# Performance work log

Hardware: AMD Instinct MI355X
Metric: run time of the kernel (lower is better)

## Reference

```python
import jax, jax.numpy as jnp
import numpy as np
from jax import lax

T, B, IN, H, L = 512, 64, 512, 1024, 2


def setup_inputs() -> dict:
    key = jax.random.key(0)
    ks = jax.random.split(key, 2 + 4 * L)
    inp = {
        'input_': jax.random.normal(ks[0], (T, B, IN), dtype=jnp.float32),
        # binary float mask for variable-length sequences
        'mask': (jax.random.uniform(ks[1], (T, B)) > 0.2).astype(jnp.float32),
    }
    k = 1.0 / np.sqrt(H)  # torch LSTMCell init range
    sizes = [(IN, H), (H, H)]
    for l in range(L):
        li, _ = sizes[l]
        base = 2 + 4 * l
        inp[f'Wih{l}'] = jax.random.uniform(ks[base + 0], (4 * H, li), minval=-k, maxval=k)
        inp[f'Whh{l}'] = jax.random.uniform(ks[base + 1], (4 * H, H), minval=-k, maxval=k)
        inp[f'bih{l}'] = jax.random.uniform(ks[base + 2], (4 * H,), minval=-k, maxval=k)
        inp[f'bhh{l}'] = jax.random.uniform(ks[base + 3], (4 * H,), minval=-k, maxval=k)
    return inp


def _lstm_layer(x, mask, Wih, Whh, bih, bhh):
    # x: [T,B,di], mask: [T,B]; precompute input-side gates for all steps
    xg = jnp.einsum('tbd,gd->tbg', x, Wih) + bih + bhh  # [T,B,4H]
    Bn = x.shape[1]
    h0 = jnp.zeros((Bn, Whh.shape[1]), x.dtype)
    c0 = jnp.zeros_like(h0)

    def step(carry, inp):
        h, c = carry
        g_x, m = inp
        gates = g_x + h @ Whh.T  # [B,4H]
        i, f, g, o = jnp.split(gates, 4, axis=-1)
        c_new = jax.nn.sigmoid(f) * c + jax.nn.sigmoid(i) * jnp.tanh(g)
        h_new = jax.nn.sigmoid(o) * jnp.tanh(c_new)
        m = m[:, None]
        h_new = h_new * m + h * (1.0 - m)
        c_new = c_new * m + c * (1.0 - m)
        return (h_new, c_new), h_new

    (h_n, c_n), out = lax.scan(step, (h0, c0), (xg, mask))
    return out, h_n, c_n


def reference(input_, mask, Wih0, Whh0, bih0, bhh0, Wih1, Whh1, bih1, bhh1):
    params = [(Wih0, Whh0, bih0, bhh0), (Wih1, Whh1, bih1, bhh1)]
    x = input_
    h_list, c_list = [], []
    for Wih, Whh, bih, bhh in params:
        x, h_n, c_n = _lstm_layer(x, mask, Wih, Whh, bih, bhh)
        h_list.append(h_n)
        c_list.append(c_n)
    return x, (jnp.stack(h_list, 0), jnp.stack(c_list, 0))
```

## Files before the change

### kernel.cpp

```cpp
#include <hip/hip_runtime.h>
#include <hip/hip_bf16.h>

#define T_ 512
#define B_ 64
#define IN_ 512
#define H_ 1024
#define G4_ 4096

typedef unsigned short u16;
typedef __attribute__((ext_vector_type(8))) short short8;
typedef __attribute__((ext_vector_type(4))) float f32x4;

__device__ __forceinline__ float sigm(float x) { return 1.0f / (1.0f + __expf(-x)); }
__device__ __forceinline__ float ftanh(float x) {
    float e = __expf(-2.0f * fabsf(x));
    float t = (1.0f - e) / (1.0f + e);
    return copysignf(t, x);
}
__device__ __forceinline__ u16 f2bf(float f) {
    unsigned int x = __float_as_uint(f);
    unsigned int r = (x + 0x7FFFu + ((x >> 16) & 1u)) >> 16;
    return (u16)r;
}

__global__ void f2b_kernel(const float* __restrict__ in, u16* __restrict__ out, int n) {
    int i = (blockIdx.x * blockDim.x + threadIdx.x) * 4;
    if (i < n) {
        float4 v = *reinterpret_cast<const float4*>(in + i);
        out[i + 0] = f2bf(v.x);
        out[i + 1] = f2bf(v.y);
        out[i + 2] = f2bf(v.z);
        out[i + 3] = f2bf(v.w);
    }
}

__global__ void bias_sum_kernel(const float* __restrict__ bih0, const float* __restrict__ bhh0,
                                const float* __restrict__ bih1, const float* __restrict__ bhh1,
                                float* __restrict__ bs0, float* __restrict__ bs1) {
    int i = blockIdx.x * blockDim.x + threadIdx.x;
    if (i < G4_) {
        bs0[i] = bih0[i] + bhh0[i];
        bs1[i] = bih1[i] + bhh1[i];
    }
}

__global__ __launch_bounds__(256) void lstm_round(
    const u16* __restrict__ in_bf,
    u16* __restrict__ out0_bf,
    const u16* __restrict__ wih0, const u16* __restrict__ whh0,
    const u16* __restrict__ wih1, const u16* __restrict__ whh1,
    const float* __restrict__ bs0, const float* __restrict__ bs1,
    const float* __restrict__ mask,
    float* __restrict__ hs,
    float* __restrict__ cs,
    u16* __restrict__ hbf,
    float* __restrict__ dout,
    int r)
{
    const int layer = blockIdx.y;
    const int t = r - layer;
    if (t < 0 || t >= T_) return;

    const int KIN = layer ? H_ : IN_;
    const u16* xt   = layer ? (out0_bf + (size_t)t * B_ * H_) : (in_bf + (size_t)t * B_ * IN_);
    const u16* Wih  = layer ? wih1 : wih0;
    const u16* Whh  = layer ? whh1 : whh0;
    const float* bsum = layer ? bs1 : bs0;
    float* h_s = hs + layer * B_ * H_;
    float* c_s = cs + layer * B_ * H_;
    const u16* hcur = hbf + ((size_t)(layer * 2 + (t & 1))) * B_ * H_;
    u16* hnxt       = hbf + ((size_t)(layer * 2 + ((t + 1) & 1))) * B_ * H_;

    __shared__ float red[4][64][32];

    const int tid  = threadIdx.x;
    const int w    = tid >> 6;
    const int lane = tid & 63;
    const int rm   = lane & 15;
    const int ks   = (lane >> 4) << 3;
    const int j0   = blockIdx.x * 8;

    f32x4 acc[4][2];
    #pragma unroll
    for (int a = 0; a < 4; ++a)
        #pragma unroll
        for (int b = 0; b < 2; ++b)
            acc[a][b] = (f32x4){0.f, 0.f, 0.f, 0.f};

    int wrow[2];
    #pragma unroll
    for (int f = 0; f < 2; ++f) {
        int cc = f * 16 + rm;
        wrow[f] = (cc >> 3) * H_ + j0 + (cc & 7);
    }

    const int nkk = (KIN + H_) >> 5;
    for (int kk = w; kk < nkk; kk += 4) {
        const int k0 = kk << 5;
        const u16* ab; int astr; const u16* wb; int wstr;
        if (k0 < KIN) { ab = xt + k0 + ks;           astr = KIN; wb = Wih + k0 + ks;           wstr = KIN; }
        else          { ab = hcur + (k0 - KIN) + ks; astr = H_;  wb = Whh + (k0 - KIN) + ks;  wstr = H_; }

        short8 afr[4], bfr[2];
        #pragma unroll
        for (int mi = 0; mi < 4; ++mi)
            afr[mi] = *reinterpret_cast<const short8*>(ab + (size_t)(mi * 16 + rm) * astr);
        #pragma unroll
        for (int f = 0; f < 2; ++f)
            bfr[f] = *reinterpret_cast<const short8*>(wb + (size_t)wrow[f] * wstr);

        #pragma unroll
        for (int mi = 0; mi < 4; ++mi)
            #pragma unroll
            for (int f = 0; f < 2; ++f)
                acc[mi][f] = __builtin_amdgcn_mfma_f32_16x16x32_bf16(afr[mi], bfr[f], acc[mi][f], 0, 0, 0);
    }

    const int rb = (lane >> 4) << 2;
    #pragma unroll
    for (int mi = 0; mi < 4; ++mi)
        #pragma unroll
        for (int f = 0; f < 2; ++f)
            #pragma unroll
            for (int rr = 0; rr < 4; ++rr)
                red[w][mi * 16 + rb + rr][f * 16 + rm] = acc[mi][f][rr];
    __syncthreads();

    const float* mt = mask + (size_t)t * B_;
    #pragma unroll
    for (int q = 0; q < 2; ++q) {
        int u  = tid * 2 + q;
        int b  = u >> 3;
        int jl = u & 7;
        int j  = j0 + jl;
        float pre[4];
        #pragma unroll
        for (int g = 0; g < 4; ++g) {
            int col = g * 8 + jl;
            pre[g] = red[0][b][col] + red[1][b][col] + red[2][b][col] + red[3][b][col]
                   + bsum[g * H_ + j];
        }
        float ig = sigm(pre[0]);
        float fg = sigm(pre[1]);
        float gg = ftanh(pre[2]);
        float og = sigm(pre[3]);
        int idx = b * H_ + j;
        float c_old = c_s[idx];
        float h_old = h_s[idx];
        float mm = mt[b];
        float c_new = fg * c_old + ig * gg;
        float h_new = og * ftanh(c_new);
        h_new = mm * h_new + (1.0f - mm) * h_old;
        c_new = mm * c_new + (1.0f - mm) * c_old;
        c_s[idx] = c_new;
        h_s[idx] = h_new;
        hnxt[idx] = f2bf(h_new);
        if (layer == 0) out0_bf[(size_t)t * B_ * H_ + idx] = f2bf(h_new);
        else            dout[(size_t)t * B_ * H_ + idx] = h_new;
    }
}

__global__ void finalize_kernel(const float* __restrict__ hs, const float* __restrict__ cs,
                                float* __restrict__ dout) {
    int i = blockIdx.x * blockDim.x + threadIdx.x;
    if (i < 2 * B_ * H_) {
        dout[(size_t)T_ * B_ * H_ + i] = hs[i];
        dout[(size_t)T_ * B_ * H_ + 2 * B_ * H_ + i] = cs[i];
    }
}

extern "C" void kernel_launch(void* const* d_in, const int* in_sizes, int n_in,
                              void* d_out, int out_size, void* d_ws, size_t ws_size,
                              hipStream_t stream) {
    const float* input_ = (const float*)d_in[0];
    const float* mask   = (const float*)d_in[1];
    const float* Wih0   = (const float*)d_in[2];
    const float* Whh0   = (const float*)d_in[3];
    const float* bih0   = (const float*)d_in[4];
    const float* bhh0   = (const float*)d_in[5];
    const float* Wih1   = (const float*)d_in[6];
    const float* Whh1   = (const float*)d_in[7];
    const float* bih1   = (const float*)d_in[8];
    const float* bhh1   = (const float*)d_in[9];
    float* dout = (float*)d_out;

    char* ws = (char*)d_ws;
    size_t off = 0;
    auto alloc = [&](size_t bytes) -> void* {
        void* p = ws + off;
        off += (bytes + 255) & ~(size_t)255;
        return p;
    };
    u16* in_bf   = (u16*)alloc((size_t)T_ * B_ * IN_ * 2);
    u16* out0_bf = (u16*)alloc((size_t)T_ * B_ * H_ * 2);
    u16* wih0    = (u16*)alloc((size_t)G4_ * IN_ * 2);
    u16* whh0    = (u16*)alloc((size_t)G4_ * H_ * 2);
    u16* wih1    = (u16*)alloc((size_t)G4_ * H_ * 2);
    u16* whh1    = (u16*)alloc((size_t)G4_ * H_ * 2);
    float* bs0   = (float*)alloc((size_t)G4_ * 4);
    float* bs1   = (float*)alloc((size_t)G4_ * 4);
    float* hs    = (float*)alloc((size_t)2 * B_ * H_ * 4);
    float* cs    = (float*)alloc((size_t)2 * B_ * H_ * 4);
    u16* hbf     = (u16*)alloc((size_t)4 * B_ * H_ * 2);

    hipMemsetAsync(hs,  0, (size_t)2 * B_ * H_ * 4, stream);
    hipMemsetAsync(cs,  0, (size_t)2 * B_ * H_ * 4, stream);
    hipMemsetAsync(hbf, 0, (size_t)4 * B_ * H_ * 2, stream);

    auto cvt = [&](const float* src, u16* dst, size_t n) {
        int blocks = (int)((n / 4 + 255) / 256);
        hipLaunchKernelGGL(f2b_kernel, dim3(blocks), dim3(256), 0, stream, src, dst, (int)n);
    };
    cvt(input_, in_bf, (size_t)T_ * B_ * IN_);
    cvt(Wih0, wih0, (size_t)G4_ * IN_);
    cvt(Whh0, whh0, (size_t)G4_ * H_);
    cvt(Wih1, wih1, (size_t)G4_ * H_);
    cvt(Whh1, whh1, (size_t)G4_ * H_);
    hipLaunchKernelGGL(bias_sum_kernel, dim3(16), dim3(256), 0, stream,
                       bih0, bhh0, bih1, bhh1, bs0, bs1);

    for (int r = 0; r <= T_; ++r) {
        hipLaunchKernelGGL(lstm_round, dim3(128, 2), dim3(256), 0, stream,
                           in_bf, out0_bf, wih0, whh0, wih1, whh1, bs0, bs1, mask,
                           hs, cs, hbf, dout, r);
    }
    hipLaunchKernelGGL(finalize_kernel, dim3((2 * B_ * H_ + 255) / 256), dim3(256), 0, stream,
                       hs, cs, dout);
}
```

Before: 10.02 ms.

## Replace per-timestep launches with persistent kernel using spin-wait counters

Replaces the 513 per-round kernel launches with one persistent kernel of 192 blocks: 64 blocks own layer 0 and 128 own layer 1. Weights stay resident in registers and h/c state is held in registers across timesteps. Blocks coordinate through global atomic counters with spin waits, and layer 1 runs pipelined behind layer 0. This removes launch overhead and repeated weight reloads, but depends on all 192 blocks being co-resident, or the spin waits deadlock. It also adds grid-wide sync latency on every step.

```diff
diff --git a/kernel.cpp b/kernel.cpp
--- a/kernel.cpp
+++ b/kernel.cpp
@@ -8,6 +8,7 @@
 #define G4_ 4096
 
 typedef unsigned short u16;
+typedef unsigned int u32;
 typedef __attribute__((ext_vector_type(8))) short short8;
 typedef __attribute__((ext_vector_type(4))) float f32x4;
 
@@ -19,8 +20,7 @@
 }
 __device__ __forceinline__ u16 f2bf(float f) {
     unsigned int x = __float_as_uint(f);
-    unsigned int r = (x + 0x7FFFu + ((x >> 16) & 1u)) >> 16;
-    return (u16)r;
+    return (u16)((x + 0x7FFFu + ((x >> 16) & 1u)) >> 16);
 }
 
 __global__ void f2b_kernel(const float* __restrict__ in, u16* __restrict__ out, int n) {
@@ -44,129 +44,188 @@
     }
 }
 
-__global__ __launch_bounds__(256) void lstm_round(
-    const u16* __restrict__ in_bf,
-    u16* __restrict__ out0_bf,
-    const u16* __restrict__ wih0, const u16* __restrict__ whh0,
-    const u16* __restrict__ wih1, const u16* __restrict__ whh1,
-    const float* __restrict__ bs0, const float* __restrict__ bs1,
-    const float* __restrict__ mask,
-    float* __restrict__ hs,
-    float* __restrict__ cs,
-    u16* __restrict__ hbf,
+__device__ __forceinline__ void spin_wait(u32* cnt, u32 target) {
+    if (threadIdx.x == 0) {
+        while (__hip_atomic_load(cnt, __ATOMIC_RELAXED, __HIP_MEMORY_SCOPE_AGENT) < target)
+            __builtin_amdgcn_s_sleep(1);
+        __threadfence();
+    }
+    __syncthreads();
+}
+
+template<int LAYER, int JTP, int XC, int HC, int NF, int NQ>
+__device__ void run_layer(
+    const u16* __restrict__ xin,
+    const u16* __restrict__ Wih, const u16* __restrict__ Whh,
+    const float* __restrict__ bsum, const float* __restrict__ mask,
+    u16* __restrict__ hsl,
+    u16* __restrict__ out_bf,
     float* __restrict__ dout,
-    int r)
+    u32* cnt_own, u32* cnt_prev, int jblk, float* red)
 {
-    const int layer = blockIdx.y;
-    const int t = r - layer;
-    if (t < 0 || t >= T_) return;
-
-    const int KIN = layer ? H_ : IN_;
-    const u16* xt   = layer ? (out0_bf + (size_t)t * B_ * H_) : (in_bf + (size_t)t * B_ * IN_);
-    const u16* Wih  = layer ? wih1 : wih0;
-    const u16* Whh  = layer ? whh1 : whh0;
-    const float* bsum = layer ? bs1 : bs0;
-    float* h_s = hs + layer * B_ * H_;
-    float* c_s = cs + layer * B_ * H_;
-    const u16* hcur = hbf + ((size_t)(layer * 2 + (t & 1))) * B_ * H_;
-    u16* hnxt       = hbf + ((size_t)(layer * 2 + ((t + 1) & 1))) * B_ * H_;
-
-    __shared__ float red[4][64][32];
+    constexpr int KSTR = LAYER ? H_ : IN_;
+    constexpr int RL = 4 * JTP + 1;
+    constexpr unsigned NJB_OWN = LAYER ? 128u : 64u;
 
     const int tid  = threadIdx.x;
     const int w    = tid >> 6;
     const int lane = tid & 63;
     const int rm   = lane & 15;
     const int ks   = (lane >> 4) << 3;
-    const int j0   = blockIdx.x * 8;
-
-    f32x4 acc[4][2];
-    #pragma unroll
-    for (int a = 0; a < 4; ++a)
-        #pragma unroll
-        for (int b = 0; b < 2; ++b)
-            acc[a][b] = (f32x4){0.f, 0.f, 0.f, 0.f};
-
-    int wrow[2];
-    #pragma unroll
-    for (int f = 0; f < 2; ++f) {
+    const int j0   = jblk * JTP;
+
+    int wrow[NF];
+    #pragma unroll
+    for (int f = 0; f < NF; ++f) {
         int cc = f * 16 + rm;
-        wrow[f] = (cc >> 3) * H_ + j0 + (cc & 7);
-    }
-
-    const int nkk = (KIN + H_) >> 5;
-    for (int kk = w; kk < nkk; kk += 4) {
-        const int k0 = kk << 5;
-        const u16* ab; int astr; const u16* wb; int wstr;
-        if (k0 < KIN) { ab = xt + k0 + ks;           astr = KIN; wb = Wih + k0 + ks;           wstr = KIN; }
-        else          { ab = hcur + (k0 - KIN) + ks; astr = H_;  wb = Whh + (k0 - KIN) + ks;  wstr = H_; }
-
-        short8 afr[4], bfr[2];
+        wrow[f] = (cc / JTP) * H_ + j0 + (cc % JTP);
+    }
+
+    short8 wx[XC][NF], wh[HC][NF];
+    #pragma unroll
+    for (int i = 0; i < XC; ++i) {
+        const int k0 = (w * XC + i) * 32;
+        #pragma unroll
+        for (int f = 0; f < NF; ++f)
+            wx[i][f] = *reinterpret_cast<const short8*>(Wih + (size_t)wrow[f] * KSTR + k0 + ks);
+    }
+    #pragma unroll
+    for (int i = 0; i < HC; ++i) {
+        const int k0 = (w * HC + i) * 32;
+        #pragma unroll
+        for (int f = 0; f < NF; ++f)
+            wh[i][f] = *reinterpret_cast<const short8*>(Whh + (size_t)wrow[f] * H_ + k0 + ks);
+    }
+
+    float bsr[NQ][4];
+    #pragma unroll
+    for (int q = 0; q < NQ; ++q) {
+        const int u = tid * NQ + q;
+        const int jl = u % JTP;
+        #pragma unroll
+        for (int g = 0; g < 4; ++g)
+            bsr[q][g] = bsum[g * H_ + j0 + jl];
+    }
+
+    float creg[NQ], hreg[NQ];
+    #pragma unroll
+    for (int q = 0; q < NQ; ++q) { creg[q] = 0.f; hreg[q] = 0.f; }
+
+    for (int t = 0; t < T_; ++t) {
+        if (LAYER == 1) spin_wait(cnt_prev, 64u * (u32)(t + 1));
+
+        const u16* xt = xin + (size_t)t * B_ * KSTR;
+        f32x4 acc[4][NF];
+        #pragma unroll
+        for (int a = 0; a < 4; ++a)
+            #pragma unroll
+            for (int f = 0; f < NF; ++f)
+                acc[a][f] = (f32x4){0.f, 0.f, 0.f, 0.f};
+
+        #pragma unroll
+        for (int i = 0; i < XC; ++i) {
+            const int k0 = (w * XC + i) * 32;
+            short8 afr[4];
+            #pragma unroll
+            for (int mi = 0; mi < 4; ++mi)
+                afr[mi] = *reinterpret_cast<const short8*>(xt + (size_t)((mi << 4) + rm) * KSTR + k0 + ks);
+            #pragma unroll
+            for (int mi = 0; mi < 4; ++mi)
+                #pragma unroll
+                for (int f = 0; f < NF; ++f)
+                    acc[mi][f] = __builtin_amdgcn_mfma_f32_16x16x32_bf16(afr[mi], wx[i][f], acc[mi][f], 0, 0, 0);
+        }
+
+        if (t > 0) {
+            spin_wait(cnt_own, NJB_OWN * (u32)t);
+            const u16* hp = hsl + (size_t)((t + 1) & 1) * B_ * H_;
+            #pragma unroll
+            for (int i = 0; i < HC; ++i) {
+                const int k0 = (w * HC + i) * 32;
+                short8 afr[4];
+                #pragma unroll
+                for (int mi = 0; mi < 4; ++mi)
+                    afr[mi] = *reinterpret_cast<const short8*>(hp + (size_t)((mi << 4) + rm) * H_ + k0 + ks);
+                #pragma unroll
+                for (int mi = 0; mi < 4; ++mi)
+                    #pragma unroll
+                    for (int f = 0; f < NF; ++f)
+                        acc[mi][f] = __builtin_amdgcn_mfma_f32_16x16x32_bf16(afr[mi], wh[i][f], acc[mi][f], 0, 0, 0);
+            }
+        }
+
+        const int rb = (lane >> 4) << 2;
         #pragma unroll
         for (int mi = 0; mi < 4; ++mi)
-            afr[mi] = *reinterpret_cast<const short8*>(ab + (size_t)(mi * 16 + rm) * astr);
-        #pragma unroll
-        for (int f = 0; f < 2; ++f)
-            bfr[f] = *reinterpret_cast<const short8*>(wb + (size_t)wrow[f] * wstr);
-
-        #pragma unroll
-        for (int mi = 0; mi < 4; ++mi)
-            #pragma unroll
-            for (int f = 0; f < 2; ++f)
-                acc[mi][f] = __builtin_amdgcn_mfma_f32_16x16x32_bf16(afr[mi], bfr[f], acc[mi][f], 0, 0, 0);
-    }
-
-    const int rb = (lane >> 4) << 2;
-    #pragma unroll
-    for (int mi = 0; mi < 4; ++mi)
-        #pragma unroll
-        for (int f = 0; f < 2; ++f)
-            #pragma unroll
-            for (int rr = 0; rr < 4; ++rr)
-                red[w][mi * 16 + rb + rr][f * 16 + rm] = acc[mi][f][rr];
-    __syncthreads();
-
-    const float* mt = mask + (size_t)t * B_;
-    #pragma unroll
-    for (int q = 0; q < 2; ++q) {
-        int u  = tid * 2 + q;
-        int b  = u >> 3;
-        int jl = u & 7;
-        int j  = j0 + jl;
-        float pre[4];
-        #pragma unroll
-        for (int g = 0; g < 4; ++g) {
-            int col = g * 8 + jl;
-            pre[g] = red[0][b][col] + red[1][b][col] + red[2][b][col] + red[3][b][col]
-                   + bsum[g * H_ + j];
+            #pragma unroll
+            for (int f = 0; f < NF; ++f)
+                #pragma unroll
+                for (int rr = 0; rr < 4; ++rr)
+                    red[((w << 6) + (mi << 4) + rb + rr) * RL + (f << 4) + rm] = acc[mi][f][rr];
+        __syncthreads();
+
+        const float* mt = mask + (size_t)t * B_;
+        u16* hw = hsl + (size_t)(t & 1) * B_ * H_;
+        #pragma unroll
+        for (int q = 0; q < NQ; ++q) {
+            const int u = tid * NQ + q;
+            const int b = u / JTP;
+            const int jl = u % JTP;
+            const int j = j0 + jl;
+            float pre[4];
+            #pragma unroll
+            for (int g = 0; g < 4; ++g) {
+                float s = 0.f;
+                #pragma unroll
+                for (int wv = 0; wv < 8; ++wv)
+                    s += red[((wv << 6) + b) * RL + g * JTP + jl];
+                pre[g] = s + bsr[q][g];
+            }
+            float ig = sigm(pre[0]);
+            float fg = sigm(pre[1]);
+            float gg = ftanh(pre[2]);
+            float og = sigm(pre[3]);
+            float c_old = creg[q], h_old = hreg[q];
+            float mm = mt[b];
+            float c_new = fg * c_old + ig * gg;
+            float h_new = og * ftanh(c_new);
+            h_new = mm * h_new + (1.f - mm) * h_old;
+            c_new = mm * c_new + (1.f - mm) * c_old;
+            creg[q] = c_new; hreg[q] = h_new;
+            const int idx = b * H_ + j;
+            hw[idx] = f2bf(h_new);
+            if (LAYER == 0) out_bf[(size_t)t * B_ * H_ + idx] = f2bf(h_new);
+            else            dout[(size_t)t * B_ * H_ + idx] = h_new;
+            if (t == T_ - 1) {
+                dout[(size_t)T_ * B_ * H_ + (size_t)LAYER * B_ * H_ + idx] = h_new;
+                dout[(size_t)T_ * B_ * H_ + (size_t)(2 + LAYER) * B_ * H_ + idx] = c_new;
+            }
         }
-        float ig = sigm(pre[0]);
-        float fg = sigm(pre[1]);
-        float gg = ftanh(pre[2]);
-        float og = sigm(pre[3]);
-        int idx = b * H_ + j;
-        float c_old = c_s[idx];
-        float h_old = h_s[idx];
-        float mm = mt[b];
-        float c_new = fg * c_old + ig * gg;
-        float h_new = og * ftanh(c_new);
-        h_new = mm * h_new + (1.0f - mm) * h_old;
-        c_new = mm * c_new + (1.0f - mm) * c_old;
-        c_s[idx] = c_new;
-        h_s[idx] = h_new;
-        hnxt[idx] = f2bf(h_new);
-        if (layer == 0) out0_bf[(size_t)t * B_ * H_ + idx] = f2bf(h_new);
-        else            dout[(size_t)t * B_ * H_ + idx] = h_new;
-    }
-}
-
-__global__ void finalize_kernel(const float* __restrict__ hs, const float* __restrict__ cs,
-                                float* __restrict__ dout) {
-    int i = blockIdx.x * blockDim.x + threadIdx.x;
-    if (i < 2 * B_ * H_) {
-        dout[(size_t)T_ * B_ * H_ + i] = hs[i];
-        dout[(size_t)T_ * B_ * H_ + 2 * B_ * H_ + i] = cs[i];
-    }
+
+        __threadfence();
+        __syncthreads();
+        if (tid == 0) atomicAdd(cnt_own, 1u);
+    }
+}
+
+__global__ __launch_bounds__(512, 2) void lstm_persist(
+    const u16* __restrict__ in_bf, u16* __restrict__ out0_bf,
+    const u16* __restrict__ wih0, const u16* __restrict__ whh0,
+    const u16* __restrict__ wih1, const u16* __restrict__ whh1,
+    const float* __restrict__ bs0, const float* __restrict__ bs1,
+    const float* __restrict__ mask, u16* __restrict__ hbf,
+    float* __restrict__ dout, u32* __restrict__ flags)
+{
+    __shared__ float red[8 * 64 * 65];
+    const int bid = blockIdx.x;
+    if (bid < 64)
+        run_layer<0, 16, 2, 4, 4, 2>(in_bf, wih0, whh0, bs0, mask,
+                                     hbf, out0_bf, dout,
+                                     flags, flags + 32, bid, red);
+    else
+        run_layer<1, 8, 4, 4, 2, 1>(out0_bf, wih1, whh1, bs1, mask,
+                                    hbf + 2 * B_ * H_, nullptr, dout,
+                                    flags + 32, flags, bid - 64, red);
 }
 
 extern "C" void kernel_launch(void* const* d_in, const int* in_sizes, int n_in,
@@ -199,13 +258,10 @@
     u16* whh1    = (u16*)alloc((size_t)G4_ * H_ * 2);
     float* bs0   = (float*)alloc((size_t)G4_ * 4);
     float* bs1   = (float*)alloc((size_t)G4_ * 4);
-    float* hs    = (float*)alloc((size_t)2 * B_ * H_ * 4);
-    float* cs    = (float*)alloc((size_t)2 * B_ * H_ * 4);
     u16* hbf     = (u16*)alloc((size_t)4 * B_ * H_ * 2);
-
-    hipMemsetAsync(hs,  0, (size_t)2 * B_ * H_ * 4, stream);
-    hipMemsetAsync(cs,  0, (size_t)2 * B_ * H_ * 4, stream);
-    hipMemsetAsync(hbf, 0, (size_t)4 * B_ * H_ * 2, stream);
+    u32* flags   = (u32*)alloc(256);
+
+    hipMemsetAsync(flags, 0, 256, stream);
 
     auto cvt = [&](const float* src, u16* dst, size_t n) {
         int blocks = (int)((n / 4 + 255) / 256);
@@ -219,11 +275,7 @@
     hipLaunchKernelGGL(bias_sum_kernel, dim3(16), dim3(256), 0, stream,
                        bih0, bhh0, bih1, bhh1, bs0, bs1);
 
-    for (int r = 0; r <= T_; ++r) {
-        hipLaunchKernelGGL(lstm_round, dim3(128, 2), dim3(256), 0, stream,
-                           in_bf, out0_bf, wih0, whh0, wih1, whh1, bs0, bs1, mask,
-                           hs, cs, hbf, dout, r);
-    }
-    hipLaunchKernelGGL(finalize_kernel, dim3((2 * B_ * H_ + 255) / 256), dim3(256), 0, stream,
-                       hs, cs, dout);
-}
+    hipLaunchKernelGGL(lstm_persist, dim3(192), dim3(512), 0, stream,
+                       in_bf, out0_bf, wih0, whh0, wih1, whh1,
+                       bs0, bs1, mask, hbf, dout, flags);
+}
```

New measurement: 27.29 ms. 172% more time.
